# Performance work log

Measured on AMD Instinct MI355X. Metric: run time of the kernel, lower is better.

The kernel has to match this reference:

```python
import jax, jax.numpy as jnp
import numpy as np

N_USERS = 100001
N_ITEMS = 200001
EMBED_DIM = 64
N_LAYERS = 3
NNZ = 3_200_000  # unique user-item interactions (before dedup)


def setup_inputs() -> dict:
    key = jax.random.key(0)
    rng = np.random.default_rng(0)
    # random bipartite interactions, deduped (dok_matrix dict semantics)
    u = rng.integers(0, N_USERS, NNZ).astype(np.int64)
    it = rng.integers(0, N_ITEMS, NNZ).astype(np.int64)
    pair = np.unique(u * N_ITEMS + it)
    u = pair // N_ITEMS
    it = pair % N_ITEMS
    N = N_USERS + N_ITEMS
    # symmetric adjacency edges: user->item and item->user blocks
    row = np.concatenate([u, it + N_USERS])
    col = np.concatenate([it + N_USERS, u])
    # L = D^-1/2 A D^-1/2 with degree from binary A, eps=1e-7 as in source
    deg = np.bincount(row, minlength=N).astype(np.float32) + 1e-7
    dinv = deg ** -0.5
    vals = (dinv[row] * dinv[col]).astype(np.float32)
    k1, k2 = jax.random.split(key)
    user_emb = jax.random.normal(k1, (N_USERS, EMBED_DIM), jnp.float32) * 0.1
    item_emb = jax.random.normal(k2, (N_ITEMS, EMBED_DIM), jnp.float32) * 0.1
    return {
        "user_emb": user_emb,
        "item_emb": item_emb,
        "row": jnp.asarray(row),
        "col": jnp.asarray(col),
        "vals": jnp.asarray(vals),
        "n_layers": N_LAYERS,
        "n_users": N_USERS,
    }


def reference(user_emb, item_emb, row, col, vals, n_layers, n_users):
    N = user_emb.shape[0] + item_emb.shape[0]
    x = jnp.concatenate([user_emb, item_emb], axis=0)  # [N, D] ego embeddings
    acc = x  # running sum fuses stack+mean over layers
    for _ in range(n_layers):
        # SpMM: out[r] += vals[e] * x[col[e]] for each edge e with row[e]=r
        x = jax.ops.segment_sum(vals[:, None] * x[col], row, num_segments=N)
        acc = acc + x
    out = acc / (n_layers + 1)  # mean over (n_layers+1) layer outputs
    return out[:n_users], out[n_users:]
```

## Files before the change

### kernel.cpp

```cpp
#include <hip/hip_runtime.h>

#define TPB 256
#define BPB 1024
#define NWG 256
#define KB_BITS 8
#define MAXB 6144

__device__ __forceinline__ unsigned int bf16pair(float a, float b) {
  unsigned int ua = __float_as_uint(a);
  ua += 0x7fffu + ((ua >> 16) & 1u);
  unsigned int ub = __float_as_uint(b);
  ub += 0x7fffu + ((ub >> 16) & 1u);
  return (ua >> 16) | (ub & 0xffff0000u);
}
__device__ __forceinline__ float bf16lo(unsigned int u) { return __uint_as_float(u << 16); }
__device__ __forceinline__ float bf16hi(unsigned int u) { return __uint_as_float(u & 0xffff0000u); }

typedef unsigned int u32x4v __attribute__((ext_vector_type(4)));
typedef float f32x4v __attribute__((ext_vector_type(4)));

__device__ __forceinline__ uint4 ntload_u4(const uint4* p) {
  u32x4v v = __builtin_nontemporal_load(reinterpret_cast<const u32x4v*>(p));
  return make_uint4(v.x, v.y, v.z, v.w);
}
__device__ __forceinline__ float4 ntload_f4(const float4* p) {
  f32x4v v = __builtin_nontemporal_load(reinterpret_cast<const f32x4v*>(p));
  return make_float4(v.x, v.y, v.z, v.w);
}
__device__ __forceinline__ void ntstore_u4(uint4* p, uint4 v) {
  u32x4v t; t.x = v.x; t.y = v.y; t.z = v.z; t.w = v.w;
  __builtin_nontemporal_store(t, reinterpret_cast<u32x4v*>(p));
}
__device__ __forceinline__ void ntstore_f4(float4* p, float4 v) {
  f32x4v t; t.x = v.x; t.y = v.y; t.z = v.z; t.w = v.w;
  __builtin_nontemporal_store(t, reinterpret_cast<f32x4v*>(p));
}

__device__ __forceinline__ int wave_incl_scan(int v, int lane) {
#pragma unroll
  for (int d = 1; d < 64; d <<= 1) {
    int t = __shfl_up(v, d, 64);
    if (lane >= d) v += t;
  }
  return v;
}

__global__ __launch_bounds__(BPB) void rp_user_and_hist(
    const int* __restrict__ row, int* __restrict__ rp, int* __restrict__ wgcnt,
    int Eh, int E, int NU, int K, int chunk, int BU) {
  extern __shared__ int hist[];
  if ((int)blockIdx.x < BU) {
    int e = blockIdx.x * BPB + threadIdx.x;
    if (e >= Eh) return;
    int r = row[e];
    int rprev = (e == 0) ? -1 : row[e - 1];
    for (int rr = rprev + 1; rr <= r; ++rr) rp[rr] = e;
    if (e == Eh - 1) {
      for (int rr = r + 1; rr < NU; ++rr) rp[rr] = Eh;
    }
  } else {
    int w = blockIdx.x - BU, tid = threadIdx.x;
    for (int b = tid; b < K; b += BPB) hist[b] = 0;
    __syncthreads();
    int s = Eh + w * chunk;
    int e_end = s + chunk; if (e_end > E) e_end = E;
    for (int e = s + tid; e < e_end; e += BPB)
      atomicAdd(&hist[(row[e] - NU) >> KB_BITS], 1);
    __syncthreads();
    for (int b = tid; b < K; b += BPB) wgcnt[b * NWG + w] = hist[b];
  }
}

__global__ __launch_bounds__(TPB) void p2a_scan(int* __restrict__ wgcnt,
                                                int* __restrict__ btot) {
  __shared__ int wsum[4];
  int b = blockIdx.x, t = threadIdx.x;
  int lane = t & 63, wv = t >> 6;
  int v = wgcnt[b * NWG + t];
  int s = wave_incl_scan(v, lane);
  if (lane == 63) wsum[wv] = s;
  __syncthreads();
  int base = 0;
#pragma unroll
  for (int w = 0; w < 4; ++w)
    if (w < wv) base += wsum[w];
  wgcnt[b * NWG + t] = base + s - v;
  if (t == TPB - 1) btot[b] = base + s;
}

__global__ __launch_bounds__(BPB) void p2b_scan(const int* __restrict__ btot,
                                                int* __restrict__ rpB,
                                                int* __restrict__ rp,
                                                int K, int Eh, int E, int N) {
  __shared__ int wsum[16];
  int t = threadIdx.x, lane = t & 63, wv = t >> 6;
  int v = (t < K) ? btot[t] : 0;
  int s = wave_incl_scan(v, lane);
  if (lane == 63) wsum[wv] = s;
  __syncthreads();
  int base = Eh;
  for (int w = 0; w < 16; ++w)
    if (w < wv) base += wsum[w];
  if (t < K) rpB[t] = base + s - v;
  if (t == 0) { rpB[K] = E; rp[N] = E; }
}

__global__ __launch_bounds__(BPB) void p3_part(
    const int* __restrict__ row, const int* __restrict__ col,
    const int* __restrict__ wgcnt, const int* __restrict__ rpB,
    unsigned int* __restrict__ evcol, int Eh, int E, int NU, int K, int chunk) {
  extern __shared__ int pos[];
  int w = blockIdx.x, tid = threadIdx.x;
  for (int b = tid; b < K; b += BPB) pos[b] = rpB[b] + wgcnt[b * NWG + w];
  __syncthreads();
  int s = Eh + w * chunk;
  int e_end = s + chunk; if (e_end > E) e_end = E;
  for (int e = s + tid; e < e_end; e += BPB) {
    int li = row[e] - NU;
    int b = li >> KB_BITS;
    int p = atomicAdd(&pos[b], 1);
    evcol[p] = ((unsigned int)(li & 255) << 24) | (unsigned int)col[e];
  }
}

__global__ __launch_bounds__(TPB) void p4_sort(unsigned int* __restrict__ evcol,
                                               const int* __restrict__ rpB,
                                               int* __restrict__ rp, int NU, int NI) {
  __shared__ unsigned int lcol[MAXB];
  __shared__ int bins[256];
  __shared__ int wsum[4];
  int b = blockIdx.x, t = threadIdx.x;
  int start = rpB[b], end = rpB[b + 1];
  int nb = end - start;
  bins[t] = 0;
  __syncthreads();
  for (int i = t; i < nb; i += TPB) {
    unsigned int v = evcol[start + i];
    lcol[i] = v;
    atomicAdd(&bins[v >> 24], 1);
  }
  __syncthreads();
  int v = bins[t];
  int lane = t & 63, wv = t >> 6;
  int s = wave_incl_scan(v, lane);
  if (lane == 63) wsum[wv] = s;
  __syncthreads();
  int base = 0;
#pragma unroll
  for (int w = 0; w < 4; ++w)
    if (w < wv) base += wsum[w];
  int excl = base + s - v;
  int item = (b << KB_BITS) + t;
  if (item < NI) rp[NU + item] = start + excl;
  bins[t] = excl;
  __syncthreads();
  for (int i = t; i < nb; i += TPB) {
    unsigned int pk = lcol[i];
    int p = atomicAdd(&bins[pk >> 24], 1);
    evcol[start + p] = pk & 0xFFFFFFu;
  }
}

__global__ void init_scaled(const float* __restrict__ u, const float* __restrict__ it,
                            const int* __restrict__ rp,
                            uint2* __restrict__ x0, int NU16, int N16) {
  int i = blockIdx.x * TPB + threadIdx.x;
  if (i >= N16) return;
  float4 v = (i < NU16) ? ntload_f4(reinterpret_cast<const float4*>(u) + i)
                        : ntload_f4(reinterpret_cast<const float4*>(it) + (i - NU16));
  int r = i >> 4;
  float deg = (float)(rp[r + 1] - rp[r]) + 1e-7f;
  float dv = rsqrtf(deg);
  x0[i] = make_uint2(bf16pair(dv * v.x, dv * v.y), bf16pair(dv * v.z, dv * v.w));
}

__device__ __forceinline__ void gather_row(const uint4* __restrict__ xv4,
                                           const unsigned int* __restrict__ ec,
                                           int start, int end, int l, float* a) {
#pragma unroll
  for (int k = 0; k < 8; ++k) a[k] = 0.f;
  int j = start;
  for (; j + 3 < end; j += 4) {
    unsigned int c0 = ec[j], c1 = ec[j + 1], c2 = ec[j + 2], c3 = ec[j + 3];
    uint4 p0 = xv4[(size_t)c0 * 8 + l];
    uint4 p1 = xv4[(size_t)c1 * 8 + l];
    uint4 p2 = xv4[(size_t)c2 * 8 + l];
    uint4 p3 = xv4[(size_t)c3 * 8 + l];
    a[0] += bf16lo(p0.x); a[1] += bf16hi(p0.x); a[2] += bf16lo(p0.y); a[3] += bf16hi(p0.y);
    a[4] += bf16lo(p0.z); a[5] += bf16hi(p0.z); a[6] += bf16lo(p0.w); a[7] += bf16hi(p0.w);
    a[0] += bf16lo(p1.x); a[1] += bf16hi(p1.x); a[2] += bf16lo(p1.y); a[3] += bf16hi(p1.y);
    a[4] += bf16lo(p1.z); a[5] += bf16hi(p1.z); a[6] += bf16lo(p1.w); a[7] += bf16hi(p1.w);
    a[0] += bf16lo(p2.x); a[1] += bf16hi(p2.x); a[2] += bf16lo(p2.y); a[3] += bf16hi(p2.y);
    a[4] += bf16lo(p2.z); a[5] += bf16hi(p2.z); a[6] += bf16lo(p2.w); a[7] += bf16hi(p2.w);
    a[0] += bf16lo(p3.x); a[1] += bf16hi(p3.x); a[2] += bf16lo(p3.y); a[3] += bf16hi(p3.y);
    a[4] += bf16lo(p3.z); a[5] += bf16hi(p3.z); a[6] += bf16lo(p3.w); a[7] += bf16hi(p3.w);
  }
  for (; j < end; ++j) {
    unsigned int c0 = ec[j];
    uint4 p = xv4[(size_t)c0 * 8 + l];
    a[0] += bf16lo(p.x); a[1] += bf16hi(p.x); a[2] += bf16lo(p.y); a[3] += bf16hi(p.y);
    a[4] += bf16lo(p.z); a[5] += bf16hi(p.z); a[6] += bf16lo(p.w); a[7] += bf16hi(p.w);
  }
}

__global__ void spmm_kernel(const unsigned int* __restrict__ x, unsigned int* __restrict__ y,
                            const int* __restrict__ rp,
                            const unsigned int* __restrict__ col_u,
                            const unsigned int* __restrict__ evcol, int N, int NU) {
  int t = blockIdx.x * TPB + threadIdx.x;
  int g = t >> 3;
  int l = t & 7;
  if (g >= N) return;
  int start = rp[g], end = rp[g + 1];
  const unsigned int* ec = (g < NU) ? col_u : evcol;
  float a[8];
  gather_row(reinterpret_cast<const uint4*>(x), ec, start, end, l, a);
  float d2 = 1.0f / ((float)(end - start) + 1e-7f);
  uint4 yo;
  yo.x = bf16pair(d2 * a[0], d2 * a[1]); yo.y = bf16pair(d2 * a[2], d2 * a[3]);
  yo.z = bf16pair(d2 * a[4], d2 * a[5]); yo.w = bf16pair(d2 * a[6], d2 * a[7]);
  ntstore_u4(reinterpret_cast<uint4*>(y) + (size_t)g * 8 + l, yo);
}

__global__ void spmm_last_kernel(const unsigned int* __restrict__ x,
                                 const int* __restrict__ rp,
                                 const unsigned int* __restrict__ col_u,
                                 const unsigned int* __restrict__ evcol,
                                 const unsigned int* __restrict__ x1,
                                 const unsigned int* __restrict__ x2,
                                 const float* __restrict__ uemb,
                                 const float* __restrict__ iemb,
                                 float* __restrict__ out, int N, int NU) {
  int t = blockIdx.x * TPB + threadIdx.x;
  int g = t >> 3;
  int l = t & 7;
  if (g >= N) return;
  int start = rp[g], end = rp[g + 1];
  const unsigned int* ec = (g < NU) ? col_u : evcol;
  float a[8];
  gather_row(reinterpret_cast<const uint4*>(x), ec, start, end, l, a);
  float deg = (float)(end - start) + 1e-7f;
  float dinv = rsqrtf(deg);
  float sq = deg * dinv;
  uint4 p1 = ntload_u4(reinterpret_cast<const uint4*>(x1) + (size_t)g * 8 + l);
  uint4 p2 = reinterpret_cast<const uint4*>(x2)[(size_t)g * 8 + l];
  const float4* ep = (g < NU)
      ? reinterpret_cast<const float4*>(uemb) + (size_t)g * 16
      : reinterpret_cast<const float4*>(iemb) + (size_t)(g - NU) * 16;
  float4 e0 = ntload_f4(ep + 2 * l), e1 = ntload_f4(ep + 2 * l + 1);
  float t0 = bf16lo(p1.x) + bf16lo(p2.x), t1 = bf16hi(p1.x) + bf16hi(p2.x);
  float t2 = bf16lo(p1.y) + bf16lo(p2.y), t3 = bf16hi(p1.y) + bf16hi(p2.y);
  float t4 = bf16lo(p1.z) + bf16lo(p2.z), t5 = bf16hi(p1.z) + bf16hi(p2.z);
  float t6 = bf16lo(p1.w) + bf16lo(p2.w), t7 = bf16hi(p1.w) + bf16hi(p2.w);
  float4 o0, o1;
  o0.x = 0.25f * (e0.x + sq * t0 + dinv * a[0]);
  o0.y = 0.25f * (e0.y + sq * t1 + dinv * a[1]);
  o0.z = 0.25f * (e0.z + sq * t2 + dinv * a[2]);
  o0.w = 0.25f * (e0.w + sq * t3 + dinv * a[3]);
  o1.x = 0.25f * (e1.x + sq * t4 + dinv * a[4]);
  o1.y = 0.25f * (e1.y + sq * t5 + dinv * a[5]);
  o1.z = 0.25f * (e1.z + sq * t6 + dinv * a[6]);
  o1.w = 0.25f * (e1.w + sq * t7 + dinv * a[7]);
  float4* op = reinterpret_cast<float4*>(out) + (size_t)g * 16;
  ntstore_f4(op + 2 * l, o0);
  ntstore_f4(op + 2 * l + 1, o1);
}

static inline char* align256(char* p) {
  return (char*)(((uintptr_t)p + 255) & ~(uintptr_t)255);
}

extern "C" void kernel_launch(void* const* d_in, const int* in_sizes, int n_in,
                              void* d_out, int out_size, void* d_ws, size_t ws_size,
                              hipStream_t stream) {
  const float* user_emb = (const float*)d_in[0];
  const float* item_emb = (const float*)d_in[1];
  const int* row = (const int*)d_in[2];
  const int* col = (const int*)d_in[3];

  const int NU = in_sizes[0] / 64;
  const int NI = in_sizes[1] / 64;
  const int N = NU + NI;
  const int E = in_sizes[2];
  const int Eh = E / 2;
  const int Eh2 = E - Eh;

  float* out = (float*)d_out;

  const int K = (NI + 255) >> KB_BITS;

  char* p = (char*)d_ws;
  unsigned int* xb[3];
  for (int k = 0; k < 3; ++k) { xb[k] = (unsigned int*)p; p = align256(p + (size_t)N * 64 * 2); }
  int* rp = (int*)p;                   p = align256(p + (size_t)(N + 1) * 4);
  int* wgcnt = (int*)p;                p = align256(p + (size_t)K * NWG * 4);
  int* btot = (int*)p;                 p = align256(p + (size_t)K * 4);
  int* rpB = (int*)p;                  p = align256(p + (size_t)(K + 1) * 4);
  unsigned int* evcol = (unsigned int*)p;

  const int N16 = N * 16;
  const int NU16 = NU * 16;
  const int chunk = (Eh2 + NWG - 1) / NWG;
  const int BU = (Eh + BPB - 1) / BPB;

  rp_user_and_hist<<<BU + NWG, BPB, K * 4, stream>>>(row, rp, wgcnt, Eh, E, NU, K, chunk, BU);
  p2a_scan<<<K, TPB, 0, stream>>>(wgcnt, btot);
  p2b_scan<<<1, BPB, 0, stream>>>(btot, rpB, rp, K, Eh, E, N);
  p3_part<<<NWG, BPB, K * 4, stream>>>(row, col, wgcnt, rpB, evcol, Eh, E, NU, K, chunk);
  p4_sort<<<K, TPB, 0, stream>>>(evcol, rpB, rp, NU, NI);

  init_scaled<<<(N16 + TPB - 1) / TPB, TPB, 0, stream>>>(user_emb, item_emb, rp,
                                                         (uint2*)xb[0], NU16, N16);

  const int spmm_blocks = (N * 8 + TPB - 1) / TPB;
  spmm_kernel<<<spmm_blocks, TPB, 0, stream>>>(xb[0], xb[1], rp,
                                               (const unsigned int*)col, evcol, N, NU);
  spmm_kernel<<<spmm_blocks, TPB, 0, stream>>>(xb[1], xb[2], rp,
                                               (const unsigned int*)col, evcol, N, NU);
  spmm_last_kernel<<<spmm_blocks, TPB, 0, stream>>>(xb[2], rp,
                                                    (const unsigned int*)col, evcol,
                                                    xb[1], xb[2], user_emb, item_emb,
                                                    out, N, NU);
}
```

Before: 585.2 us.

## Fuse CSR build and init into single cooperative kernel with grid syncs

Replaces six preprocessing kernels (user row-pointer build, histogram, two scans, partition, per-bucket sort, scaled bf16 init) with one cooperative kernel of 256 blocks of 1024 threads that uses grid.sync between phases. The goal is to remove launch overhead and the gaps between small kernels. The cost is less parallelism in some phases: the bucket sort now runs with only 256 blocks looping over K buckets, and the init and user-rowptr loops are grid-strided. Grid barriers also add their own latency.

New measurement: 771.9 us. 1.32x slower.

```diff
diff --git a/kernel.cpp b/kernel.cpp
--- a/kernel.cpp
+++ b/kernel.cpp
@@ -1,8 +1,11 @@
 #include <hip/hip_runtime.h>
+#include <hip/hip_cooperative_groups.h>
+
+namespace cg = cooperative_groups;
 
 #define TPB 256
-#define BPB 1024
-#define NWG 256
+#define CGRID 256
+#define CTPB 1024
 #define KB_BITS 8
 #define MAXB 6144
 
@@ -45,133 +48,128 @@
   return v;
 }
 
-__global__ __launch_bounds__(BPB) void rp_user_and_hist(
-    const int* __restrict__ row, int* __restrict__ rp, int* __restrict__ wgcnt,
-    int Eh, int E, int NU, int K, int chunk, int BU) {
-  extern __shared__ int hist[];
-  if ((int)blockIdx.x < BU) {
-    int e = blockIdx.x * BPB + threadIdx.x;
-    if (e >= Eh) return;
+__global__ __launch_bounds__(CTPB) void csr_fused(
+    const int* __restrict__ row, const int* __restrict__ col,
+    const float* __restrict__ uemb, const float* __restrict__ iemb,
+    int* __restrict__ rp, int* __restrict__ wgcnt, int* __restrict__ btot,
+    int* __restrict__ rpB, unsigned int* __restrict__ evcol,
+    uint2* __restrict__ x0,
+    int Eh, int E, int NU, int NI, int N, int K, int chunk, int NU16, int N16) {
+  cg::grid_group grid = cg::this_grid();
+  __shared__ int sh[1024];
+  __shared__ unsigned int lcol[MAXB];
+  __shared__ int bins[256];
+  __shared__ int wsum[16];
+  const int b0 = blockIdx.x, t = threadIdx.x;
+  const int lane = t & 63, wv = t >> 6;
+
+  for (int e = b0 * CTPB + t; e < Eh; e += CGRID * CTPB) {
     int r = row[e];
     int rprev = (e == 0) ? -1 : row[e - 1];
     for (int rr = rprev + 1; rr <= r; ++rr) rp[rr] = e;
     if (e == Eh - 1) {
       for (int rr = r + 1; rr < NU; ++rr) rp[rr] = Eh;
     }
-  } else {
-    int w = blockIdx.x - BU, tid = threadIdx.x;
-    for (int b = tid; b < K; b += BPB) hist[b] = 0;
-    __syncthreads();
-    int s = Eh + w * chunk;
-    int e_end = s + chunk; if (e_end > E) e_end = E;
-    for (int e = s + tid; e < e_end; e += BPB)
-      atomicAdd(&hist[(row[e] - NU) >> KB_BITS], 1);
-    __syncthreads();
-    for (int b = tid; b < K; b += BPB) wgcnt[b * NWG + w] = hist[b];
-  }
-}
-
-__global__ __launch_bounds__(TPB) void p2a_scan(int* __restrict__ wgcnt,
-                                                int* __restrict__ btot) {
-  __shared__ int wsum[4];
-  int b = blockIdx.x, t = threadIdx.x;
-  int lane = t & 63, wv = t >> 6;
-  int v = wgcnt[b * NWG + t];
-  int s = wave_incl_scan(v, lane);
-  if (lane == 63) wsum[wv] = s;
+  }
+  for (int i = t; i < K; i += CTPB) sh[i] = 0;
   __syncthreads();
-  int base = 0;
+  const int s0 = Eh + b0 * chunk;
+  const int e1 = (s0 + chunk < E) ? s0 + chunk : E;
+  for (int e = s0 + t; e < e1; e += CTPB)
+    atomicAdd(&sh[(row[e] - NU) >> KB_BITS], 1);
+  __syncthreads();
+  for (int i = t; i < K; i += CTPB) wgcnt[i * CGRID + b0] = sh[i];
+  grid.sync();
+
+  for (int b = b0; b < K; b += CGRID) {
+    int v = 0, s = 0;
+    if (t < CGRID) {
+      v = wgcnt[b * CGRID + t];
+      s = wave_incl_scan(v, lane);
+      if (lane == 63) wsum[wv] = s;
+    }
+    __syncthreads();
+    if (t < CGRID) {
+      int base = 0;
 #pragma unroll
-  for (int w = 0; w < 4; ++w)
-    if (w < wv) base += wsum[w];
-  wgcnt[b * NWG + t] = base + s - v;
-  if (t == TPB - 1) btot[b] = base + s;
-}
-
-__global__ __launch_bounds__(BPB) void p2b_scan(const int* __restrict__ btot,
-                                                int* __restrict__ rpB,
-                                                int* __restrict__ rp,
-                                                int K, int Eh, int E, int N) {
-  __shared__ int wsum[16];
-  int t = threadIdx.x, lane = t & 63, wv = t >> 6;
-  int v = (t < K) ? btot[t] : 0;
-  int s = wave_incl_scan(v, lane);
-  if (lane == 63) wsum[wv] = s;
+      for (int w = 0; w < CGRID / 64; ++w)
+        if (w < wv) base += wsum[w];
+      wgcnt[b * CGRID + t] = base + s - v;
+      if (t == CGRID - 1) btot[b] = base + s;
+    }
+    __syncthreads();
+  }
+  grid.sync();
+
+  if (b0 == 0) {
+    int v = (t < K) ? btot[t] : 0;
+    int s = wave_incl_scan(v, lane);
+    if (lane == 63) wsum[wv] = s;
+    __syncthreads();
+    int base = Eh;
+    for (int w = 0; w < 16; ++w)
+      if (w < wv) base += wsum[w];
+    if (t < K) rpB[t] = base + s - v;
+    if (t == 0) { rpB[K] = E; rp[N] = E; }
+  }
+  grid.sync();
+
+  for (int i = t; i < K; i += CTPB) sh[i] = rpB[i] + wgcnt[i * CGRID + b0];
   __syncthreads();
-  int base = Eh;
-  for (int w = 0; w < 16; ++w)
-    if (w < wv) base += wsum[w];
-  if (t < K) rpB[t] = base + s - v;
-  if (t == 0) { rpB[K] = E; rp[N] = E; }
-}
-
-__global__ __launch_bounds__(BPB) void p3_part(
-    const int* __restrict__ row, const int* __restrict__ col,
-    const int* __restrict__ wgcnt, const int* __restrict__ rpB,
-    unsigned int* __restrict__ evcol, int Eh, int E, int NU, int K, int chunk) {
-  extern __shared__ int pos[];
-  int w = blockIdx.x, tid = threadIdx.x;
-  for (int b = tid; b < K; b += BPB) pos[b] = rpB[b] + wgcnt[b * NWG + w];
-  __syncthreads();
-  int s = Eh + w * chunk;
-  int e_end = s + chunk; if (e_end > E) e_end = E;
-  for (int e = s + tid; e < e_end; e += BPB) {
+  for (int e = s0 + t; e < e1; e += CTPB) {
     int li = row[e] - NU;
     int b = li >> KB_BITS;
-    int p = atomicAdd(&pos[b], 1);
+    int p = atomicAdd(&sh[b], 1);
     evcol[p] = ((unsigned int)(li & 255) << 24) | (unsigned int)col[e];
   }
-}
-
-__global__ __launch_bounds__(TPB) void p4_sort(unsigned int* __restrict__ evcol,
-                                               const int* __restrict__ rpB,
-                                               int* __restrict__ rp, int NU, int NI) {
-  __shared__ unsigned int lcol[MAXB];
-  __shared__ int bins[256];
-  __shared__ int wsum[4];
-  int b = blockIdx.x, t = threadIdx.x;
-  int start = rpB[b], end = rpB[b + 1];
-  int nb = end - start;
-  bins[t] = 0;
-  __syncthreads();
-  for (int i = t; i < nb; i += TPB) {
-    unsigned int v = evcol[start + i];
-    lcol[i] = v;
-    atomicAdd(&bins[v >> 24], 1);
-  }
-  __syncthreads();
-  int v = bins[t];
-  int lane = t & 63, wv = t >> 6;
-  int s = wave_incl_scan(v, lane);
-  if (lane == 63) wsum[wv] = s;
-  __syncthreads();
-  int base = 0;
+  grid.sync();
+
+  for (int b = b0; b < K; b += CGRID) {
+    int start = rpB[b], end = rpB[b + 1];
+    int nb = end - start;
+    if (t < 256) bins[t] = 0;
+    __syncthreads();
+    for (int i = t; i < nb; i += CTPB) {
+      unsigned int v = evcol[start + i];
+      lcol[i] = v;
+      atomicAdd(&bins[v >> 24], 1);
+    }
+    __syncthreads();
+    int v2 = 0, s2 = 0;
+    if (t < 256) {
+      v2 = bins[t];
+      s2 = wave_incl_scan(v2, lane);
+      if (lane == 63) wsum[wv] = s2;
+    }
+    __syncthreads();
+    if (t < 256) {
+      int base = 0;
 #pragma unroll
-  for (int w = 0; w < 4; ++w)
-    if (w < wv) base += wsum[w];
-  int excl = base + s - v;
-  int item = (b << KB_BITS) + t;
-  if (item < NI) rp[NU + item] = start + excl;
-  bins[t] = excl;
-  __syncthreads();
-  for (int i = t; i < nb; i += TPB) {
-    unsigned int pk = lcol[i];
-    int p = atomicAdd(&bins[pk >> 24], 1);
-    evcol[start + p] = pk & 0xFFFFFFu;
-  }
-}
-
-__global__ void init_scaled(const float* __restrict__ u, const float* __restrict__ it,
-                            const int* __restrict__ rp,
-                            uint2* __restrict__ x0, int NU16, int N16) {
-  int i = blockIdx.x * TPB + threadIdx.x;
-  if (i >= N16) return;
-  float4 v = (i < NU16) ? ntload_f4(reinterpret_cast<const float4*>(u) + i)
-                        : ntload_f4(reinterpret_cast<const float4*>(it) + (i - NU16));
-  int r = i >> 4;
-  float deg = (float)(rp[r + 1] - rp[r]) + 1e-7f;
-  float dv = rsqrtf(deg);
-  x0[i] = make_uint2(bf16pair(dv * v.x, dv * v.y), bf16pair(dv * v.z, dv * v.w));
+      for (int w = 0; w < 4; ++w)
+        if (w < wv) base += wsum[w];
+      int excl = base + s2 - v2;
+      int item = (b << KB_BITS) + t;
+      if (item < NI) rp[NU + item] = start + excl;
+      bins[t] = excl;
+    }
+    __syncthreads();
+    for (int i = t; i < nb; i += CTPB) {
+      unsigned int pk = lcol[i];
+      int p = atomicAdd(&bins[pk >> 24], 1);
+      evcol[start + p] = pk & 0xFFFFFFu;
+    }
+    __syncthreads();
+  }
+  grid.sync();
+
+  for (int i = b0 * CTPB + t; i < N16; i += CGRID * CTPB) {
+    float4 v = (i < NU16) ? ntload_f4(reinterpret_cast<const float4*>(uemb) + i)
+                          : ntload_f4(reinterpret_cast<const float4*>(iemb) + (i - NU16));
+    int r = i >> 4;
+    float deg = (float)(rp[r + 1] - rp[r]) + 1e-7f;
+    float dv = rsqrtf(deg);
+    x0[i] = make_uint2(bf16pair(dv * v.x, dv * v.y), bf16pair(dv * v.z, dv * v.w));
+  }
 }
 
 __device__ __forceinline__ void gather_row(const uint4* __restrict__ xv4,
@@ -273,10 +271,10 @@
 extern "C" void kernel_launch(void* const* d_in, const int* in_sizes, int n_in,
                               void* d_out, int out_size, void* d_ws, size_t ws_size,
                               hipStream_t stream) {
+  const int* row = (const int*)d_in[2];
+  const int* col = (const int*)d_in[3];
   const float* user_emb = (const float*)d_in[0];
   const float* item_emb = (const float*)d_in[1];
-  const int* row = (const int*)d_in[2];
-  const int* col = (const int*)d_in[3];
 
   const int NU = in_sizes[0] / 64;
   const int NI = in_sizes[1] / 64;
@@ -293,24 +291,28 @@
   unsigned int* xb[3];
   for (int k = 0; k < 3; ++k) { xb[k] = (unsigned int*)p; p = align256(p + (size_t)N * 64 * 2); }
   int* rp = (int*)p;                   p = align256(p + (size_t)(N + 1) * 4);
-  int* wgcnt = (int*)p;                p = align256(p + (size_t)K * NWG * 4);
+  int* wgcnt = (int*)p;                p = align256(p + (size_t)K * CGRID * 4);
   int* btot = (int*)p;                 p = align256(p + (size_t)K * 4);
   int* rpB = (int*)p;                  p = align256(p + (size_t)(K + 1) * 4);
   unsigned int* evcol = (unsigned int*)p;
 
   const int N16 = N * 16;
   const int NU16 = NU * 16;
-  const int chunk = (Eh2 + NWG - 1) / NWG;
-  const int BU = (Eh + BPB - 1) / BPB;
-
-  rp_user_and_hist<<<BU + NWG, BPB, K * 4, stream>>>(row, rp, wgcnt, Eh, E, NU, K, chunk, BU);
-  p2a_scan<<<K, TPB, 0, stream>>>(wgcnt, btot);
-  p2b_scan<<<1, BPB, 0, stream>>>(btot, rpB, rp, K, Eh, E, N);
-  p3_part<<<NWG, BPB, K * 4, stream>>>(row, col, wgcnt, rpB, evcol, Eh, E, NU, K, chunk);
-  p4_sort<<<K, TPB, 0, stream>>>(evcol, rpB, rp, NU, NI);
-
-  init_scaled<<<(N16 + TPB - 1) / TPB, TPB, 0, stream>>>(user_emb, item_emb, rp,
-                                                         (uint2*)xb[0], NU16, N16);
+  const int chunk = (Eh2 + CGRID - 1) / CGRID;
+
+  {
+    uint2* x0 = (uint2*)xb[0];
+    int Eh_ = Eh, E_ = E, NU_ = NU, NI_ = NI, N_ = N, K_ = K, chunk_ = chunk,
+        NU16_ = NU16, N16_ = N16;
+    const int* row_ = row; const int* col_ = col;
+    const float* ue_ = user_emb; const float* ie_ = item_emb;
+    int* rp_ = rp; int* wg_ = wgcnt; int* bt_ = btot; int* rb_ = rpB;
+    unsigned int* ev_ = evcol;
+    void* args[] = {&row_, &col_, &ue_, &ie_, &rp_, &wg_, &bt_, &rb_, &ev_, &x0,
+                    &Eh_, &E_, &NU_, &NI_, &N_, &K_, &chunk_, &NU16_, &N16_};
+    hipLaunchCooperativeKernel((const void*)csr_fused, dim3(CGRID), dim3(CTPB),
+                               args, 0, stream);
+  }
 
   const int spmm_blocks = (N * 8 + TPB - 1) / TPB;
   spmm_kernel<<<spmm_blocks, TPB, 0, stream>>>(xb[0], xb[1], rp,
```
